# Performance work log

Hardware: AMD Instinct MI355X
Metric: run time of the kernel (lower is better)

The kernel has to match this reference:

```python
import jax, jax.numpy as jnp
import numpy as np

DIM = 1024
N_HEADS = 16
N_KV = 4
HEAD_DIM = DIM // N_HEADS          # 64
GROUP = N_HEADS // N_KV            # 4
KV_DIM = N_KV * HEAD_DIM           # 256
B, S = 2, 2048


def setup_inputs() -> dict:
    key = jax.random.key(0)
    ks = jax.random.split(key, 5)
    scale = 1.0 / np.sqrt(DIM)
    return {
        "x": jax.random.normal(ks[0], (B, S, DIM), dtype=jnp.float32),
        "W_qkv": jax.random.normal(ks[1], (DIM, DIM + 2 * KV_DIM), dtype=jnp.float32) * scale,
        "b_qkv": jnp.zeros((DIM + 2 * KV_DIM,), dtype=jnp.float32),
        "W_out": jax.random.normal(ks[2], (DIM, DIM), dtype=jnp.float32) * scale,
        "b_out": jnp.zeros((DIM,), dtype=jnp.float32),
    }


def reference(x, W_qkv, b_qkv, W_out, b_out):
    b, s, d = x.shape
    qkv = x @ W_qkv + b_qkv                                   # [b, s, dim + 2*kv_dim]
    q, k, v = jnp.split(qkv, [DIM, DIM + KV_DIM], axis=-1)
    # q: [b, n_kv, group, s, hd]; k, v: [b, n_kv, s, hd]
    q = q.reshape(b, s, N_HEADS, HEAD_DIM).transpose(0, 2, 1, 3)
    q = q.reshape(b, N_KV, GROUP, s, HEAD_DIM)
    k = k.reshape(b, s, N_KV, HEAD_DIM).transpose(0, 2, 1, 3)
    v = v.reshape(b, s, N_KV, HEAD_DIM).transpose(0, 2, 1, 3)
    scores = jnp.einsum("bkgsd,bktd->bkgst", q, k) / np.sqrt(HEAD_DIM)
    causal = jnp.tril(jnp.ones((s, s), dtype=bool))           # [s, s]
    scores = jnp.where(causal, scores, -jnp.inf)
    attn = jax.nn.softmax(scores, axis=-1)                    # dropout = 0 (eval)
    y = jnp.einsum("bkgst,bktd->bkgsd", attn, v)              # [b, n_kv, g, s, hd]
    y = y.reshape(b, N_HEADS, s, HEAD_DIM).transpose(0, 2, 1, 3).reshape(b, s, d)
    return y @ W_out + b_out
```

## Files before the change

kernel.cpp:

```cpp
#include <hip/hip_runtime.h>
#include <cstdint>
#include <cstddef>

typedef __bf16 bf16x8 __attribute__((ext_vector_type(8)));
typedef __bf16 bf16x4 __attribute__((ext_vector_type(4)));
typedef float  f32x4  __attribute__((ext_vector_type(4)));
typedef short  s16x4  __attribute__((ext_vector_type(4)));

#define DIMD 1024
#define SEQ  2048
#define NB   2
#define NH   16
#define HD   64
#define QKVN 1536
#define VOFF 1280
#define VSTR 2080
#define CSC  0.18033688011112042f

#if __has_builtin(__builtin_amdgcn_mfma_f32_16x16x16bf16_1k)
#define HAS_MFMA16 1
#else
#define HAS_MFMA16 0
#endif

typedef __attribute__((address_space(1))) const void* as1_cvp;
typedef __attribute__((address_space(3))) void* as3_vp;
#define GLL16(g, l) __builtin_amdgcn_global_load_lds((as1_cvp)(const void*)(g), (as3_vp)(void*)(l), 16, 0, 0)

__global__ void cvt_f32_bf16(const float* __restrict__ in, __bf16* __restrict__ out, int n4) {
    int i = blockIdx.x * blockDim.x + threadIdx.x;
    if (i >= n4) return;
    float4 v = reinterpret_cast<const float4*>(in)[i];
    bf16x4 o;
    o[0] = (__bf16)v.x; o[1] = (__bf16)v.y; o[2] = (__bf16)v.z; o[3] = (__bf16)v.w;
    reinterpret_cast<bf16x4*>(out)[i] = o;
}

__global__ void transpose_cvt(const float* __restrict__ in, __bf16* __restrict__ out, int R, int C) {
    __shared__ float t[32][33];
    int bx = blockIdx.x * 32;
    int by = blockIdx.y * 32;
    int tx = threadIdx.x, ty = threadIdx.y;
#pragma unroll
    for (int i = 0; i < 32; i += 8)
        t[ty + i][tx] = in[(size_t)(by + ty + i) * C + bx + tx];
    __syncthreads();
#pragma unroll
    for (int i = 0; i < 32; i += 8)
        out[(size_t)(bx + ty + i) * R + by + tx] = (__bf16)t[tx][ty + i];
}

__global__ void transpose_v(const __bf16* __restrict__ qkv, __bf16* __restrict__ vtg) {
    __shared__ __bf16 t[32][34];
    const int z = blockIdx.z;
    const int b = z >> 2, kh = z & 3;
    const int s0 = blockIdx.x * 32, d0 = blockIdx.y * 32;
    const int tx = threadIdx.x, ty = threadIdx.y;
    const __bf16* src = qkv + (size_t)b * SEQ * QKVN + VOFF + kh * HD;
#pragma unroll
    for (int i = 0; i < 32; i += 8)
        t[ty + i][tx] = src[(size_t)(s0 + ty + i) * QKVN + d0 + tx];
    __syncthreads();
    __bf16* dst = vtg + ((size_t)z * HD + d0) * VSTR + s0;
#pragma unroll
    for (int i = 0; i < 32; i += 8)
        dst[(size_t)(ty + i) * VSTR + tx] = t[tx][ty + i];
}

template<int OUT_BF16, int QSCALE>
__global__ __launch_bounds__(256) void gemm_bf16(
    const __bf16* __restrict__ A, const __bf16* __restrict__ Bt,
    const float* __restrict__ bias, void* __restrict__ Cout,
    int M, int N, int K, int nx)
{
    __shared__ __bf16 Als[128 * 32];
    __shared__ __bf16 Bls[64 * 32];
    const int tid  = threadIdx.x;
    const int lane = tid & 63;
    const int wave = tid >> 6;
    const int lo = lane & 15, hi = lane >> 4;

    const int lin = blockIdx.x;
    const int cpx = gridDim.x >> 3;
    const int swz = (lin & 7) * cpx + (lin >> 3);
    const int bm = (swz / nx) * 128, bn = (swz % nx) * 64;
    const int wr = (wave >> 1) * 64, wc = (wave & 1) * 32;

    const __bf16* gA = A  + (size_t)(bm + wave * 16 + (lane >> 2)) * K + (lane & 3) * 8;
    const __bf16* gB = Bt + (size_t)(bn + wave * 16 + (lane >> 2)) * K + (lane & 3) * 8;
    __bf16* lA = &Als[wave * 16 * 32];
    __bf16* lB = &Bls[wave * 16 * 32];

    f32x4 acc[4][2] = {};

    for (int k0 = 0; k0 < K; k0 += 32) {
        __syncthreads();
        GLL16(gA + k0,                  lA);
        GLL16(gA + k0 + (size_t)64 * K, lA + 2048);
        GLL16(gB + k0,                  lB);
        __syncthreads();

        bf16x8 af[4], bfr[2];
#pragma unroll
        for (int i = 0; i < 4; i++)
            af[i] = *reinterpret_cast<const bf16x8*>(&Als[(wr + i * 16 + lo) * 32 + hi * 8]);
#pragma unroll
        for (int j = 0; j < 2; j++)
            bfr[j] = *reinterpret_cast<const bf16x8*>(&Bls[(wc + j * 16 + lo) * 32 + hi * 8]);
#pragma unroll
        for (int i = 0; i < 4; i++)
#pragma unroll
            for (int j = 0; j < 2; j++)
                acc[i][j] = __builtin_amdgcn_mfma_f32_16x16x32_bf16(af[i], bfr[j], acc[i][j], 0, 0, 0);
    }

#pragma unroll
    for (int j = 0; j < 2; j++) {
        int col = bn + wc + j * 16 + lo;
        float bv = bias[col];
#pragma unroll
        for (int i = 0; i < 4; i++) {
            int row0 = bm + wr + i * 16 + hi * 4;
#pragma unroll
            for (int rr = 0; rr < 4; rr++) {
                float v = acc[i][j][rr] + bv;
                if (QSCALE && col < DIMD) v *= CSC;
                if (OUT_BF16) ((__bf16*)Cout)[(size_t)(row0 + rr) * N + col] = (__bf16)v;
                else          ((float* )Cout)[(size_t)(row0 + rr) * N + col] = v;
            }
        }
    }
}

__global__ __launch_bounds__(1024, 8) void attn_fwd(
    const __bf16* __restrict__ qkv, const __bf16* __restrict__ vt, __bf16* __restrict__ y)
{
    __shared__ __bf16 Ka[2][8192];
    __shared__ __bf16 Va[2][8192];
#if !HAS_MFMA16
    __shared__ __bf16 Pls[16][16][72];
#endif
    const int tid  = threadIdx.x;
    const int wave = tid >> 6, lane = tid & 63;
    const int lo = lane & 15, hi = lane >> 4;
    const int head = wave & 3, tt = (wave >> 2) & 1, par = wave >> 3;

    const int bid = blockIdx.x;
    const int z  = bid & 7;
    const int b  = z >> 2, kh = z & 3;
    const int c2 = bid >> 3;
    const int p  = (c2 < 32) ? c2 : 95 - c2;
    const int h  = kh * 4 + head;

    const int T  = tt ? 127 - p : p;
    const int qw = T * 16;
    const int cT = (T >> 2) + 1;
    const int cMax = ((127 - p) >> 2) + 1;
    const int S = (cMax + 1) >> 1;

    const __bf16* base = qkv + (size_t)b * SEQ * QKVN;
    const __bf16* qp = base + h * HD;
    const __bf16* kp = base + DIMD + kh * HD;
    const __bf16* vp = vt + (size_t)z * HD * VSTR;

    const int krow = lane >> 3;
    const __bf16* kst = kp + (size_t)(wave * 8 + krow) * QKVN + ((lane & 7) ^ krow) * 8;
    const int vrow = lane >> 4;
    const int vsu  = (lane & 15) ^ (4 * (wave & 1) + vrow);
    const __bf16* vst = vp + (size_t)(wave * 4 + vrow) * VSTR + vsu * 8;
    __bf16* kd = &Ka[0][wave * 512];
    __bf16* vd = &Va[0][wave * 512];

#define STAGE(s, buf)                                        \
    do {                                                     \
        GLL16(kst + (size_t)(s) * 128 * QKVN, kd + (buf) * 8192); \
        GLL16(vst + (s) * 128,                vd + (buf) * 8192); \
    } while (0)

    const int xk = lo & 7;
    const int u0 = (hi ^ xk) * 8;
    const int u1 = ((hi + 4) ^ xk) * 8;
#if HAS_MFMA16
    int voff[4];
#pragma unroll
    for (int ks = 0; ks < 4; ks++)
        voff[ks] = (((par * 8 + ks * 2 + (hi >> 1)) ^ xk) << 3) + (hi & 1) * 4;
#endif

    bf16x8 bQ0 = *reinterpret_cast<const bf16x8*>(qp + (size_t)(qw + lo) * QKVN + hi * 8);
    bf16x8 bQ1 = *reinterpret_cast<const bf16x8*>(qp + (size_t)(qw + lo) * QKVN + 32 + hi * 8);

    f32x4 accO[4] = {};
    f32x4 ssv = {0.f, 0.f, 0.f, 0.f};

    STAGE(0, 0);
    __syncthreads();

    int cur = 0;
    for (int s = 0; s < S; ++s) {
        if (s + 1 < S) STAGE(s + 1, cur ^ 1);

        const int ce = 2 * s + par;
        if (ce < cT) {
            const int kbase = ce * 64;
            const bool dT = (ce == cT - 1);
            const __bf16* Kb = &Ka[cur][(size_t)par * 64 * 64];
            const __bf16* Vb = &Va[cur][0];

#pragma unroll
            for (int ks = 0; ks < 4; ks++) {
                const __bf16* Kr = Kb + (ks * 16 + lo) * 64;
                bf16x8 aK0 = *reinterpret_cast<const bf16x8*>(Kr + u0);
                bf16x8 aK1 = *reinterpret_cast<const bf16x8*>(Kr + u1);
                f32x4 sv = {0.f, 0.f, 0.f, 0.f};
                sv = __builtin_amdgcn_mfma_f32_16x16x32_bf16(aK0, bQ0, sv, 0, 0, 0);
                sv = __builtin_amdgcn_mfma_f32_16x16x32_bf16(aK1, bQ1, sv, 0, 0, 0);

                bf16x4 pk;
#pragma unroll
                for (int r = 0; r < 4; r++) {
                    float e = exp2f(sv[r]);
                    if (dT && (kbase + ks * 16 + hi * 4 + r > qw + lo)) e = 0.0f;
                    ssv[r] += e;
                    pk[r] = (__bf16)e;
                }

#if HAS_MFMA16
#pragma unroll
                for (int f = 0; f < 4; f++) {
                    bf16x4 vf = *reinterpret_cast<const bf16x4*>(&Vb[(f * 16 + lo) * 128] + voff[ks]);
                    accO[f] = __builtin_amdgcn_mfma_f32_16x16x16bf16_1k(
                        __builtin_bit_cast(s16x4, vf), __builtin_bit_cast(s16x4, pk),
                        accO[f], 0, 0, 0);
                }
#else
                *reinterpret_cast<bf16x4*>(&Pls[wave][lo][ks * 16 + hi * 4]) = pk;
#endif
            }

#if !HAS_MFMA16
#pragma unroll
            for (int k2 = 0; k2 < 2; k2++) {
                const int uv = ((par * 8 + k2 * 4 + hi) ^ xk) * 8;
                bf16x8 pA = *reinterpret_cast<const bf16x8*>(&Pls[wave][lo][k2 * 32 + hi * 8]);
#pragma unroll
                for (int f = 0; f < 4; f++) {
                    bf16x8 vB = *reinterpret_cast<const bf16x8*>(&Vb[(f * 16 + lo) * 128] + uv);
                    accO[f] = __builtin_amdgcn_mfma_f32_16x16x32_bf16(pA, vB, accO[f], 0, 0, 0);
                }
            }
#endif
        }

        __syncthreads();
        cur ^= 1;
    }
#undef STAGE

    float ss = (ssv[0] + ssv[1]) + (ssv[2] + ssv[3]);

    float* comb = (float*)&Ka[0][0];
    const int sidx = ((wave & 7) * 64 + lane) * 20;
    if (par == 1) {
#pragma unroll
        for (int f = 0; f < 4; f++)
            *reinterpret_cast<f32x4*>(&comb[sidx + f * 4]) = accO[f];
        comb[sidx + 16] = ss;
    }
    __syncthreads();
    if (par == 0) {
#pragma unroll
        for (int f = 0; f < 4; f++)
            accO[f] += *reinterpret_cast<const f32x4*>(&comb[sidx + f * 4]);
        ss += comb[sidx + 16];

#if HAS_MFMA16
        ss += __shfl_xor(ss, 16);
        ss += __shfl_xor(ss, 32);
        float inv = 1.0f / ss;
        const size_t yb = (size_t)(b * SEQ + qw + lo) * DIMD + h * HD + hi * 4;
#pragma unroll
        for (int f = 0; f < 4; f++) {
            bf16x4 o;
#pragma unroll
            for (int r = 0; r < 4; r++) o[r] = (__bf16)(accO[f][r] * inv);
            *reinterpret_cast<bf16x4*>(&y[yb + f * 16]) = o;
        }
#else
        ss += __shfl_xor(ss, 16);
        ss += __shfl_xor(ss, 32);
#pragma unroll
        for (int r = 0; r < 4; r++) {
            float sr = __shfl(ss, hi * 4 + r);
            float inv = 1.0f / sr;
            int q = qw + hi * 4 + r;
#pragma unroll
            for (int f = 0; f < 4; f++)
                y[(size_t)(b * SEQ + q) * DIMD + h * HD + f * 16 + lo] = (__bf16)(accO[f][r] * inv);
        }
#endif
    }
}

extern "C" void kernel_launch(void* const* d_in, const int* in_sizes, int n_in,
                              void* d_out, int out_size, void* d_ws, size_t ws_size,
                              hipStream_t stream) {
    const float* x    = (const float*)d_in[0];
    const float* Wqkv = (const float*)d_in[1];
    const float* bqkv = (const float*)d_in[2];
    const float* Wout = (const float*)d_in[3];
    const float* bout = (const float*)d_in[4];
    float* out = (float*)d_out;

    char* ws = (char*)d_ws;
    __bf16* xb    = (__bf16*)(ws);
    __bf16* wqkvT = (__bf16*)(ws + ((size_t)8  << 20));
    __bf16* woutT = (__bf16*)(ws + ((size_t)11 << 20));
    __bf16* qkvb  = (__bf16*)(ws + ((size_t)13 << 20));
    __bf16* vtg   = wqkvT;
    __bf16* yb    = xb;

    const int M = NB * SEQ;

    cvt_f32_bf16<<<(M * DIMD / 4 + 255) / 256, 256, 0, stream>>>(x, xb, M * DIMD / 4);
    transpose_cvt<<<dim3(QKVN / 32, DIMD / 32), dim3(32, 8), 0, stream>>>(Wqkv, wqkvT, DIMD, QKVN);
    transpose_cvt<<<dim3(DIMD / 32, DIMD / 32), dim3(32, 8), 0, stream>>>(Wout, woutT, DIMD, DIMD);

    gemm_bf16<1, 1><<<(M / 128) * (QKVN / 64), 256, 0, stream>>>(
        xb, wqkvT, bqkv, qkvb, M, QKVN, DIMD, QKVN / 64);

    transpose_v<<<dim3(SEQ / 32, HD / 32, NB * 4), dim3(32, 8), 0, stream>>>(qkvb, vtg);

    attn_fwd<<<512, 1024, 0, stream>>>(qkvb, vtg, yb);

    gemm_bf16<0, 0><<<(M / 128) * (DIMD / 64), 256, 0, stream>>>(
        yb, woutT, bout, out, M, DIMD, DIMD, DIMD / 64);
}
```

Measured before the change: 112.9 us.

## Process two query heads per wave in attention to reuse K/V fragments

The attention kernel now has each wave handle two heads of the same KV group, so every K fragment and V fragment read from shared memory feeds two MFMA chains. Blocks shrink from 1024 to 512 threads, and each wave stages twice as many K/V rows per step. The non-MFMA16 fallback path is removed. The aim is to halve LDS reads per MFMA and add independent MFMA work to hide latency, at the cost of higher register pressure and fewer waves sharing each block's load work.

```diff
diff --git a/kernel.cpp b/kernel.cpp
--- a/kernel.cpp
+++ b/kernel.cpp
@@ -16,12 +16,6 @@
 #define VOFF 1280
 #define VSTR 2080
 #define CSC  0.18033688011112042f
-
-#if __has_builtin(__builtin_amdgcn_mfma_f32_16x16x16bf16_1k)
-#define HAS_MFMA16 1
-#else
-#define HAS_MFMA16 0
-#endif
 
 typedef __attribute__((address_space(1))) const void* as1_cvp;
 typedef __attribute__((address_space(3))) void* as3_vp;
@@ -132,25 +126,22 @@
     }
 }
 
-__global__ __launch_bounds__(1024, 8) void attn_fwd(
+__global__ __launch_bounds__(512, 4) void attn_fwd(
     const __bf16* __restrict__ qkv, const __bf16* __restrict__ vt, __bf16* __restrict__ y)
 {
     __shared__ __bf16 Ka[2][8192];
     __shared__ __bf16 Va[2][8192];
-#if !HAS_MFMA16
-    __shared__ __bf16 Pls[16][16][72];
-#endif
     const int tid  = threadIdx.x;
     const int wave = tid >> 6, lane = tid & 63;
     const int lo = lane & 15, hi = lane >> 4;
-    const int head = wave & 3, tt = (wave >> 2) & 1, par = wave >> 3;
+    const int hp = wave & 1, tt = (wave >> 1) & 1, par = wave >> 2;
 
     const int bid = blockIdx.x;
     const int z  = bid & 7;
     const int b  = z >> 2, kh = z & 3;
     const int c2 = bid >> 3;
     const int p  = (c2 < 32) ? c2 : 95 - c2;
-    const int h  = kh * 4 + head;
+    const int h0 = kh * 4 + hp * 2;
 
     const int T  = tt ? 127 - p : p;
     const int qw = T * 16;
@@ -159,39 +150,44 @@
     const int S = (cMax + 1) >> 1;
 
     const __bf16* base = qkv + (size_t)b * SEQ * QKVN;
-    const __bf16* qp = base + h * HD;
+    const __bf16* qp = base + h0 * HD;
     const __bf16* kp = base + DIMD + kh * HD;
     const __bf16* vp = vt + (size_t)z * HD * VSTR;
 
     const int krow = lane >> 3;
-    const __bf16* kst = kp + (size_t)(wave * 8 + krow) * QKVN + ((lane & 7) ^ krow) * 8;
+    const __bf16* kst = kp + (size_t)(wave * 16 + krow) * QKVN + ((lane & 7) ^ krow) * 8;
     const int vrow = lane >> 4;
-    const int vsu  = (lane & 15) ^ (4 * (wave & 1) + vrow);
-    const __bf16* vst = vp + (size_t)(wave * 4 + vrow) * VSTR + vsu * 8;
-    __bf16* kd = &Ka[0][wave * 512];
-    __bf16* vd = &Va[0][wave * 512];
-
-#define STAGE(s, buf)                                        \
-    do {                                                     \
-        GLL16(kst + (size_t)(s) * 128 * QKVN, kd + (buf) * 8192); \
-        GLL16(vst + (s) * 128,                vd + (buf) * 8192); \
+    const __bf16* vst0 = vp + (size_t)(wave * 8 + vrow) * VSTR + (((lane & 15) ^ vrow) * 8);
+    const __bf16* vst1 = vp + (size_t)(wave * 8 + 4 + vrow) * VSTR + (((lane & 15) ^ (vrow + 4)) * 8);
+    __bf16* kd = &Ka[0][wave * 1024];
+    __bf16* vd = &Va[0][wave * 1024];
+
+#define STAGE(s, buf)                                                       \
+    do {                                                                    \
+        const size_t ko = (size_t)(s) * 128 * QKVN;                         \
+        const int    vo = (s) * 128;                                        \
+        GLL16(kst + ko,                     kd + (buf) * 8192);             \
+        GLL16(kst + ko + (size_t)8 * QKVN,  kd + (buf) * 8192 + 512);       \
+        GLL16(vst0 + vo,                    vd + (buf) * 8192);             \
+        GLL16(vst1 + vo,                    vd + (buf) * 8192 + 512);       \
     } while (0)
 
     const int xk = lo & 7;
     const int u0 = (hi ^ xk) * 8;
     const int u1 = ((hi + 4) ^ xk) * 8;
-#if HAS_MFMA16
     int voff[4];
 #pragma unroll
     for (int ks = 0; ks < 4; ks++)
         voff[ks] = (((par * 8 + ks * 2 + (hi >> 1)) ^ xk) << 3) + (hi & 1) * 4;
-#endif
-
-    bf16x8 bQ0 = *reinterpret_cast<const bf16x8*>(qp + (size_t)(qw + lo) * QKVN + hi * 8);
-    bf16x8 bQ1 = *reinterpret_cast<const bf16x8*>(qp + (size_t)(qw + lo) * QKVN + 32 + hi * 8);
-
-    f32x4 accO[4] = {};
-    f32x4 ssv = {0.f, 0.f, 0.f, 0.f};
+
+    const __bf16* qrow = qp + (size_t)(qw + lo) * QKVN + hi * 8;
+    bf16x8 bQ0a = *reinterpret_cast<const bf16x8*>(qrow);
+    bf16x8 bQ1a = *reinterpret_cast<const bf16x8*>(qrow + 32);
+    bf16x8 bQ0b = *reinterpret_cast<const bf16x8*>(qrow + HD);
+    bf16x8 bQ1b = *reinterpret_cast<const bf16x8*>(qrow + HD + 32);
+
+    f32x4 accA[4] = {}, accB[4] = {};
+    f32x4 ssva = {0.f, 0.f, 0.f, 0.f}, ssvb = {0.f, 0.f, 0.f, 0.f};
 
     STAGE(0, 0);
     __syncthreads();
@@ -204,7 +200,7 @@
         if (ce < cT) {
             const int kbase = ce * 64;
             const bool dT = (ce == cT - 1);
-            const __bf16* Kb = &Ka[cur][(size_t)par * 64 * 64];
+            const __bf16* Kb = &Ka[cur][par * 4096];
             const __bf16* Vb = &Va[cur][0];
 
 #pragma unroll
@@ -212,44 +208,33 @@
                 const __bf16* Kr = Kb + (ks * 16 + lo) * 64;
                 bf16x8 aK0 = *reinterpret_cast<const bf16x8*>(Kr + u0);
                 bf16x8 aK1 = *reinterpret_cast<const bf16x8*>(Kr + u1);
-                f32x4 sv = {0.f, 0.f, 0.f, 0.f};
-                sv = __builtin_amdgcn_mfma_f32_16x16x32_bf16(aK0, bQ0, sv, 0, 0, 0);
-                sv = __builtin_amdgcn_mfma_f32_16x16x32_bf16(aK1, bQ1, sv, 0, 0, 0);
-
-                bf16x4 pk;
+
+                f32x4 sa = {0.f, 0.f, 0.f, 0.f}, sb = {0.f, 0.f, 0.f, 0.f};
+                sa = __builtin_amdgcn_mfma_f32_16x16x32_bf16(aK0, bQ0a, sa, 0, 0, 0);
+                sb = __builtin_amdgcn_mfma_f32_16x16x32_bf16(aK0, bQ0b, sb, 0, 0, 0);
+                sa = __builtin_amdgcn_mfma_f32_16x16x32_bf16(aK1, bQ1a, sa, 0, 0, 0);
+                sb = __builtin_amdgcn_mfma_f32_16x16x32_bf16(aK1, bQ1b, sb, 0, 0, 0);
+
+                bf16x4 pka, pkb;
 #pragma unroll
                 for (int r = 0; r < 4; r++) {
-                    float e = exp2f(sv[r]);
-                    if (dT && (kbase + ks * 16 + hi * 4 + r > qw + lo)) e = 0.0f;
-                    ssv[r] += e;
-                    pk[r] = (__bf16)e;
+                    float ea = exp2f(sa[r]);
+                    float eb = exp2f(sb[r]);
+                    if (dT && (kbase + ks * 16 + hi * 4 + r > qw + lo)) { ea = 0.0f; eb = 0.0f; }
+                    ssva[r] += ea;  ssvb[r] += eb;
+                    pka[r] = (__bf16)ea;  pkb[r] = (__bf16)eb;
                 }
 
-#if HAS_MFMA16
 #pragma unroll
                 for (int f = 0; f < 4; f++) {
                     bf16x4 vf = *reinterpret_cast<const bf16x4*>(&Vb[(f * 16 + lo) * 128] + voff[ks]);
-                    accO[f] = __builtin_amdgcn_mfma_f32_16x16x16bf16_1k(
-                        __builtin_bit_cast(s16x4, vf), __builtin_bit_cast(s16x4, pk),
-                        accO[f], 0, 0, 0);
-                }
-#else
-                *reinterpret_cast<bf16x4*>(&Pls[wave][lo][ks * 16 + hi * 4]) = pk;
-#endif
-            }
-
-#if !HAS_MFMA16
-#pragma unroll
-            for (int k2 = 0; k2 < 2; k2++) {
-                const int uv = ((par * 8 + k2 * 4 + hi) ^ xk) * 8;
-                bf16x8 pA = *reinterpret_cast<const bf16x8*>(&Pls[wave][lo][k2 * 32 + hi * 8]);
-#pragma unroll
-                for (int f = 0; f < 4; f++) {
-                    bf16x8 vB = *reinterpret_cast<const bf16x8*>(&Vb[(f * 16 + lo) * 128] + uv);
-                    accO[f] = __builtin_amdgcn_mfma_f32_16x16x32_bf16(pA, vB, accO[f], 0, 0, 0);
+                    s16x4 vfi = __builtin_bit_cast(s16x4, vf);
+                    accA[f] = __builtin_amdgcn_mfma_f32_16x16x16bf16_1k(
+                        vfi, __builtin_bit_cast(s16x4, pka), accA[f], 0, 0, 0);
+                    accB[f] = __builtin_amdgcn_mfma_f32_16x16x16bf16_1k(
+                        vfi, __builtin_bit_cast(s16x4, pkb), accB[f], 0, 0, 0);
                 }
             }
-#endif
         }
 
         __syncthreads();
@@ -257,48 +242,45 @@
     }
 #undef STAGE
 
-    float ss = (ssv[0] + ssv[1]) + (ssv[2] + ssv[3]);
+    float ssa = (ssva[0] + ssva[1]) + (ssva[2] + ssva[3]);
+    float ssb = (ssvb[0] + ssvb[1]) + (ssvb[2] + ssvb[3]);
 
     float* comb = (float*)&Ka[0][0];
-    const int sidx = ((wave & 7) * 64 + lane) * 20;
+    const int sidx = ((wave & 3) * 64 + lane) * 40;
     if (par == 1) {
 #pragma unroll
-        for (int f = 0; f < 4; f++)
-            *reinterpret_cast<f32x4*>(&comb[sidx + f * 4]) = accO[f];
-        comb[sidx + 16] = ss;
+        for (int f = 0; f < 4; f++) {
+            *reinterpret_cast<f32x4*>(&comb[sidx + f * 4])      = accA[f];
+            *reinterpret_cast<f32x4*>(&comb[sidx + 16 + f * 4]) = accB[f];
+        }
+        comb[sidx + 32] = ssa;
+        comb[sidx + 33] = ssb;
     }
     __syncthreads();
     if (par == 0) {
 #pragma unroll
-        for (int f = 0; f < 4; f++)
-            accO[f] += *reinterpret_cast<const f32x4*>(&comb[sidx + f * 4]);
-        ss += comb[sidx + 16];
-
-#if HAS_MFMA16
-        ss += __shfl_xor(ss, 16);
-        ss += __shfl_xor(ss, 32);
-        float inv = 1.0f / ss;
-        const size_t yb = (size_t)(b * SEQ + qw + lo) * DIMD + h * HD + hi * 4;
-#pragma unroll
         for (int f = 0; f < 4; f++) {
-            bf16x4 o;
-#pragma unroll
-            for (int r = 0; r < 4; r++) o[r] = (__bf16)(accO[f][r] * inv);
-            *reinterpret_cast<bf16x4*>(&y[yb + f * 16]) = o;
-        }
-#else
-        ss += __shfl_xor(ss, 16);
-        ss += __shfl_xor(ss, 32);
-#pragma unroll
-        for (int r = 0; r < 4; r++) {
-            float sr = __shfl(ss, hi * 4 + r);
-            float inv = 1.0f / sr;
-            int q = qw + hi * 4 + r;
-#pragma unroll
-            for (int f = 0; f < 4; f++)
-                y[(size_t)(b * SEQ + q) * DIMD + h * HD + f * 16 + lo] = (__bf16)(accO[f][r] * inv);
-        }
-#endif
+            accA[f] += *reinterpret_cast<const f32x4*>(&comb[sidx + f * 4]);
+            accB[f] += *reinterpret_cast<const f32x4*>(&comb[sidx + 16 + f * 4]);
+        }
+        ssa += comb[sidx + 32];
+        ssb += comb[sidx + 33];
+
+        ssa += __shfl_xor(ssa, 16);  ssa += __shfl_xor(ssa, 32);
+        ssb += __shfl_xor(ssb, 16);  ssb += __shfl_xor(ssb, 32);
+        float inva = 1.0f / ssa, invb = 1.0f / ssb;
+        const size_t yb = (size_t)(b * SEQ + qw + lo) * DIMD + h0 * HD + hi * 4;
+#pragma unroll
+        for (int f = 0; f < 4; f++) {
+            bf16x4 oa, ob;
+#pragma unroll
+            for (int r = 0; r < 4; r++) {
+                oa[r] = (__bf16)(accA[f][r] * inva);
+                ob[r] = (__bf16)(accB[f][r] * invb);
+            }
+            *reinterpret_cast<bf16x4*>(&y[yb + f * 16])      = oa;
+            *reinterpret_cast<bf16x4*>(&y[yb + HD + f * 16]) = ob;
+        }
     }
 }
 
@@ -331,7 +313,7 @@
 
     transpose_v<<<dim3(SEQ / 32, HD / 32, NB * 4), dim3(32, 8), 0, stream>>>(qkvb, vtg);
 
-    attn_fwd<<<512, 1024, 0, stream>>>(qkvb, vtg, yb);
+    attn_fwd<<<512, 512, 0, stream>>>(qkvb, vtg, yb);
 
     gemm_bf16<0, 0><<<(M / 128) * (DIMD / 64), 256, 0, stream>>>(
         yb, woutT, bout, out, M, DIMD, DIMD, DIMD / 64);
```

New measurement: 119.7 us. 1.06x slower.
